# Kernel optimization log

Hardware: AMD Instinct MI355X
Metric: run time of the kernel (lower is better)

## Reference

```python
import jax, jax.numpy as jnp
import numpy as np
from functools import partial

VOCAB = 1000
HID = 512
EPS = 1e-3  # Keras BatchNorm default epsilon


def _conv1d(x, w, stride):
    # x: [B,T,C_in], w: [K,C_in,C_out]
    return jax.lax.conv_general_dilated(x, w, window_strides=(stride,), padding='SAME',
                                        dimension_numbers=('NWC', 'WIO', 'NWC'))


def setup_inputs() -> dict:
    key = jax.random.key(0)
    ks = jax.random.split(key, 8)
    s = lambda *sh: 1.0 / np.sqrt(sh[-2] if len(sh) > 1 else sh[-1])
    return {
        'x': jax.random.normal(ks[0], (32, 1600, 80), jnp.float32),
        'y_true': jax.random.randint(ks[1], (32, 201), 0, VOCAB),
        'bn_gamma': jnp.ones((80,), jnp.float32),
        'bn_beta': jnp.zeros((80,), jnp.float32),
        'conv0_w': jax.random.normal(ks[2], (5, 80, 512), jnp.float32) * 0.05,
        'conv0_b': jnp.zeros((512,), jnp.float32),
        'tcr_w': jax.random.normal(ks[3], (4, 5, 512, 512), jnp.float32) * 0.02,
        'tcr_b': jnp.zeros((4, 512), jnp.float32),
        'gru_kernel': jax.random.normal(ks[4], (VOCAB, 3 * HID), jnp.float32) * 0.03,
        'gru_rec_kernel': jax.random.normal(ks[5], (HID, 3 * HID), jnp.float32) * 0.04,
        'gru_bias': jnp.zeros((2, 3 * HID), jnp.float32),
        'fc_w': jax.random.normal(ks[6], (2 * HID, VOCAB), jnp.float32) * 0.03,
        'fc_b': jnp.zeros((VOCAB,), jnp.float32),
    }


def reference(x, y_true, bn_gamma, bn_beta, conv0_w, conv0_b, tcr_w, tcr_b,
              gru_kernel, gru_rec_kernel, gru_bias, fc_w, fc_b):
    # ---- Encoder ----
    # BatchNorm (training mode: batch statistics over batch & time)
    mean = jnp.mean(x, axis=(0, 1))
    var = jnp.var(x, axis=(0, 1))
    h = (x - mean) * jax.lax.rsqrt(var + EPS) * bn_gamma + bn_beta
    # strided Conv1D + relu -> [B, T=800, 512]
    h = jax.nn.relu(_conv1d(h, conv0_w, 2) + conv0_b)
    # Temporal conv residual blocks: out = relu(conv(x)) + x
    for i in range(tcr_w.shape[0]):
        h = jax.nn.relu(_conv1d(h, tcr_w[i], 1) + tcr_b[i]) + h
    enc = h  # [B, T, D]
    B = enc.shape[0]

    # ---- Decoder (teacher forcing, training branch) ----
    y_oh = jax.nn.one_hot(y_true, VOCAB, dtype=jnp.float32)  # [B, U+1, V]
    inputs = jnp.transpose(y_oh[:, :-1, :], (1, 0, 2))       # [U, B, V]
    bi, br = gru_bias[0], gru_bias[1]

    def step(hstate, y_u):
        # Keras GRUCell (reset_after=True)
        mx = y_u @ gru_kernel + bi
        mh = hstate @ gru_rec_kernel + br
        xz, xr, xh = jnp.split(mx, 3, axis=-1)
        hz, hr, hh = jnp.split(mh, 3, axis=-1)
        z = jax.nn.sigmoid(xz + hz)
        r = jax.nn.sigmoid(xr + hr)
        cand = jnp.tanh(xh + r * hh)
        h_new = z * hstate + (1.0 - z) * cand
        # Dot-product attention over encoder states
        scores = jnp.einsum('bd,btd->bt', h_new, enc)
        alpha = jax.nn.softmax(scores, axis=-1)
        ctx = jnp.einsum('bt,btd->bd', alpha, enc)
        # output projection with softmax activation
        y_pred = jax.nn.softmax(jnp.concatenate([h_new, ctx], axis=1) @ fc_w + fc_b, axis=-1)
        return h_new, y_pred

    h0 = jnp.zeros((B, HID), jnp.float32)
    _, outs = jax.lax.scan(step, h0, inputs)  # [U, B, V]
    return jnp.transpose(outs, (1, 0, 2))     # [B, U, V]
```

## Files before the change

### kernel.cpp

```cpp
#include <hip/hip_runtime.h>
#include <cstdint>

typedef _Float16 f16;
typedef __attribute__((ext_vector_type(2))) _Float16 f16x2;
typedef __attribute__((ext_vector_type(8))) _Float16 f16x8;
typedef __attribute__((ext_vector_type(4))) float f32x4;
typedef __attribute__((ext_vector_type(2))) float f32x2;
typedef __attribute__((ext_vector_type(8))) unsigned short us8;
typedef __attribute__((ext_vector_type(4))) int i32x4;

#define NB   32
#define TIN  1600
#define CIN  80
#define TOUT 800
#define DH   512
#define NV   1000
#define NU   200
#define TXP  1604
#define THP  804
#define EPSB 1e-3f
#define EWG  248

__device__ __forceinline__ void st_sys_f16(f16* p, float v)
{
    f16 h = (f16)v;
    short s; __builtin_memcpy(&s, &h, 2);
    int si = (int)s;
    asm volatile("global_store_short %0, %1, off sc0 sc1"
                 :: "v"(p), "v"(si) : "memory");
}

__device__ __forceinline__ void poll_h16(const f16* base, f16x8 v[16])
{
    while (true) {
        asm volatile(
            "global_load_dwordx4 %0, %16, off sc1\n\t"
            "global_load_dwordx4 %1, %16, off offset:64 sc1\n\t"
            "global_load_dwordx4 %2, %16, off offset:128 sc1\n\t"
            "global_load_dwordx4 %3, %16, off offset:192 sc1\n\t"
            "global_load_dwordx4 %4, %16, off offset:256 sc1\n\t"
            "global_load_dwordx4 %5, %16, off offset:320 sc1\n\t"
            "global_load_dwordx4 %6, %16, off offset:384 sc1\n\t"
            "global_load_dwordx4 %7, %16, off offset:448 sc1\n\t"
            "global_load_dwordx4 %8, %16, off offset:512 sc1\n\t"
            "global_load_dwordx4 %9, %16, off offset:576 sc1\n\t"
            "global_load_dwordx4 %10, %16, off offset:640 sc1\n\t"
            "global_load_dwordx4 %11, %16, off offset:704 sc1\n\t"
            "global_load_dwordx4 %12, %16, off offset:768 sc1\n\t"
            "global_load_dwordx4 %13, %16, off offset:832 sc1\n\t"
            "global_load_dwordx4 %14, %16, off offset:896 sc1\n\t"
            "global_load_dwordx4 %15, %16, off offset:960 sc1\n\t"
            "s_waitcnt vmcnt(0)"
            : "=&v"(v[0]), "=&v"(v[1]), "=&v"(v[2]), "=&v"(v[3]),
              "=&v"(v[4]), "=&v"(v[5]), "=&v"(v[6]), "=&v"(v[7]),
              "=&v"(v[8]), "=&v"(v[9]), "=&v"(v[10]), "=&v"(v[11]),
              "=&v"(v[12]), "=&v"(v[13]), "=&v"(v[14]), "=&v"(v[15])
            : "v"(base)
            : "memory");
        f16x8 s0 = v[0] + v[1],   s1 = v[2] + v[3];
        f16x8 s2 = v[4] + v[5],   s3 = v[6] + v[7];
        f16x8 s4 = v[8] + v[9],   s5 = v[10] + v[11];
        f16x8 s6 = v[12] + v[13], s7 = v[14] + v[15];
        s0 += s1; s2 += s3; s4 += s5; s6 += s7;
        s0 += s2; s4 += s6; s0 += s4;
        float r = (float)s0[0] + (float)s0[1] + (float)s0[2] + (float)s0[3]
                + (float)s0[4] + (float)s0[5] + (float)s0[6] + (float)s0[7];
        if (!__any(r != r)) return;
        __builtin_amdgcn_s_sleep(1);
    }
}

__device__ __forceinline__ float fast_tanh(float x)
{
    return 1.f - 2.f / (__expf(2.f * x) + 1.f);
}

__global__ void init_zero(float* gsum, float* gsumsq,
                          int* lcnt, f16* xpad, f16* hbufA, f16* hbufB,
                          f16* Hc)
{
    int tid = blockIdx.x * 256 + threadIdx.x;
    int stride = gridDim.x * 256;
    if (blockIdx.x == 0) {
        if (threadIdx.x < 80) { gsum[threadIdx.x] = 0.f; gsumsq[threadIdx.x] = 0.f; }
        if (threadIdx.x >= 128 && threadIdx.x < 136) lcnt[threadIdx.x - 128] = 0;
    }
    for (int i = tid; i < NB * 4 * CIN; i += stride) {
        int b = i / (4 * CIN), rr = (i / CIN) % 4, c = i % CIN;
        int row = (rr == 0) ? 0 : (1600 + rr);
        xpad[((long)b * TXP + row) * CIN + c] = (f16)0.f;
    }
    for (int i = tid; i < 2 * NB * 4 * DH; i += stride) {
        int q = i; int buf = q / (NB * 4 * DH); q %= NB * 4 * DH;
        int b = q / (4 * DH); int rr = (q / DH) % 4; int dd = q % DH;
        int row = (rr < 2) ? rr : (800 + rr);
        f16* hb = buf ? hbufB : hbufA;
        hb[((long)b * THP + row) * DH + dd] = (f16)0.f;
    }
    us8 sent;
#pragma unroll
    for (int e = 0; e < 8; e++) sent[e] = 0x7FFFu;
    for (int i = tid; i < 6400 * 64; i += stride)
        *(us8*)&Hc[(long)(i >> 6) * 1024 + (i & 63) * 8] = sent;
}

__global__ void transpose_f32_f16(const float* __restrict__ in, int R, int C,
                                  f16* __restrict__ out, int outRows, int outCols)
{
    __shared__ float t[32][33];
    int c0 = blockIdx.x * 32, r0 = blockIdx.y * 32;
    int x = threadIdx.x & 31, y = threadIdx.x >> 5;
    for (int i = y; i < 32; i += 8) {
        int r = r0 + i, c = c0 + x;
        t[i][x] = (r < R && c < C) ? in[(long)r * C + c] : 0.0f;
    }
    __syncthreads();
    for (int i = y; i < 32; i += 8) {
        int orow = c0 + i, ocol = r0 + x;
        if (orow < outRows && ocol < outCols)
            out[(long)orow * outCols + ocol] = (f16)t[x][i];
    }
}

__global__ void bn_stats(const float* __restrict__ x, float* gsum, float* gsumsq)
{
    __shared__ float ls[240], ls2[240];
    const float* base = x + (long)blockIdx.x * 200 * CIN;
    int tid = threadIdx.x;
    if (tid < 240) {
        int c = tid % 80, rg = tid / 80;
        float s = 0.f, s2 = 0.f;
        for (int r = rg; r < 200; r += 3) {
            float v = base[r * CIN + c];
            s += v; s2 += v * v;
        }
        ls[tid] = s; ls2[tid] = s2;
    }
    __syncthreads();
    if (tid < 80) {
        atomicAdd(&gsum[tid],   ls[tid] + ls[tid + 80] + ls[tid + 160]);
        atomicAdd(&gsumsq[tid], ls2[tid] + ls2[tid + 80] + ls2[tid + 160]);
    }
}

__global__ void bn_apply(const float* __restrict__ x, const float* __restrict__ gsum,
                         const float* __restrict__ gsumsq, const float* __restrict__ gamma,
                         const float* __restrict__ beta, f16* __restrict__ xpad)
{
    long idx = (long)blockIdx.x * 256 + threadIdx.x;
    if (idx >= (long)NB * TIN * CIN) return;
    int c = (int)(idx % CIN);
    long bt = idx / CIN;
    int t = (int)(bt % TIN); int b = (int)(bt / TIN);
    float mean = gsum[c] * (1.f / 51200.f);
    float var  = gsumsq[c] * (1.f / 51200.f) - mean * mean;
    float sc = gamma[c] * rsqrtf(var + EPSB);
    float sh = beta[c] - mean * sc;
    xpad[((long)b * TXP + t + 1) * CIN + c] = (f16)(x[idx] * sc + sh);
}

template<int MODE>
__launch_bounds__(256)
__global__ void gemm16(const f16* __restrict__ Ab, long strideA, long slabA,
                       const f16* __restrict__ Bb, long strideB, long slabB,
                       int M, int N, int Kchunks,
                       const float* __restrict__ bias,
                       float* __restrict__ outF)
{
    __shared__ f16 As[64][72];
    __shared__ f16 Bs[128][72];
    const int b = blockIdx.z;
    const f16* Abase = Ab + (long)b * slabA;
    const f16* Bbase = Bb + (long)b * slabB;
    const int m0 = blockIdx.x * 64, n0 = blockIdx.y * 128;
    const int tid = threadIdx.x;
    const int lane = tid & 63, wv = tid >> 6;
    const int lm = lane & 15, lk = lane >> 4;

    f32x4 vzero = {0.f, 0.f, 0.f, 0.f};
    f32x4 acc[4][2];
#pragma unroll
    for (int i = 0; i < 4; i++) { acc[i][0] = vzero; acc[i][1] = vzero; }

    const int srow = tid >> 3, scol = (tid & 7) * 8;

    for (int kc = 0; kc < Kchunks; kc++) {
        int kb = kc * 64;
#pragma unroll
        for (int p = 0; p < 2; p++) {
            int r = srow + p * 32;
            int m = m0 + r; if (m > M - 1) m = M - 1;
            *(us8*)&As[r][scol] = *(const us8*)(Abase + (long)m * strideA + kb + scol);
        }
#pragma unroll
        for (int p = 0; p < 4; p++) {
            int r = srow + p * 32;
            int n = n0 + r; if (n > N - 1) n = N - 1;
            *(us8*)&Bs[r][scol] = *(const us8*)(Bbase + (long)n * strideB + kb + scol);
        }
        __syncthreads();
#pragma unroll
        for (int ks = 0; ks < 2; ks++) {
            f16x8 af[4], bf[2];
#pragma unroll
            for (int mt = 0; mt < 4; mt++)
                af[mt] = *(const f16x8*)&As[mt * 16 + lm][ks * 32 + lk * 8];
#pragma unroll
            for (int nt = 0; nt < 2; nt++)
                bf[nt] = *(const f16x8*)&Bs[wv * 32 + nt * 16 + lm][ks * 32 + lk * 8];
#pragma unroll
            for (int mt = 0; mt < 4; mt++)
#pragma unroll
                for (int nt = 0; nt < 2; nt++)
                    acc[mt][nt] = __builtin_amdgcn_mfma_f32_16x16x32_f16(af[mt], bf[nt], acc[mt][nt], 0, 0, 0);
        }
        __syncthreads();
    }
#pragma unroll
    for (int mt = 0; mt < 4; mt++) {
#pragma unroll
        for (int nt = 0; nt < 2; nt++) {
            int n = n0 + wv * 32 + nt * 16 + lm;
#pragma unroll
            for (int reg = 0; reg < 4; reg++) {
                int m = m0 + mt * 16 + lk * 4 + reg;
                if (m >= M || n >= N) continue;
                float v = acc[mt][nt][reg];
                if (MODE == 2) {
                    outF[((long)b * NU + m) * 800 + n] = v;
                } else {
                    v += bias[n];
                    int u = m >> 5, bb = m & 31;
                    outF[((long)bb * NU + u) * 1000 + n] = v;
                }
            }
        }
    }
}

__device__ void enc_layer(int eb, int tid,
                          const f16* __restrict__ Ab, long strideA, long slabA,
                          const f16* __restrict__ Bb, long strideB,
                          int Kchunks, const float* __restrict__ bias,
                          const f16* __restrict__ resid, f16* __restrict__ outH,
                          long slabRO, f16 As[][72], f16 Bs[][72])
{
    const int lane = tid & 63, wv = tid >> 6;
    const int lm = lane & 15, lk = lane >> 4;
    const int srow = tid >> 3, scol = (tid & 7) * 8;
    f32x4 vzero = {0.f, 0.f, 0.f, 0.f};

    for (int t = eb; t < 1664; t += EWG) {
        int b = t / 52, rem = t - b * 52;
        int m0 = (rem >> 2) * 64, n0 = (rem & 3) * 128;
        const f16* Abase = Ab + (long)b * slabA;

        f32x4 acc[4][2];
#pragma unroll
        for (int i = 0; i < 4; i++) { acc[i][0] = vzero; acc[i][1] = vzero; }

        for (int kc = 0; kc < Kchunks; kc++) {
            int kb = kc * 64;
#pragma unroll
            for (int p = 0; p < 2; p++) {
                int r = srow + p * 32;
                int m = m0 + r; if (m > 799) m = 799;
                *(us8*)&As[r][scol] = *(const us8*)(Abase + (long)m * strideA + kb + scol);
            }
#pragma unroll
            for (int p = 0; p < 4; p++) {
                int r = srow + p * 32;
                *(us8*)&Bs[r][scol] = *(const us8*)(Bb + (long)(n0 + r) * strideB + kb + scol);
            }
            __syncthreads();
#pragma unroll
            for (int ks = 0; ks < 2; ks++) {
                f16x8 af[4], bf[2];
#pragma unroll
                for (int mt = 0; mt < 4; mt++)
                    af[mt] = *(const f16x8*)&As[mt * 16 + lm][ks * 32 + lk * 8];
#pragma unroll
                for (int nt = 0; nt < 2; nt++)
                    bf[nt] = *(const f16x8*)&Bs[wv * 32 + nt * 16 + lm][ks * 32 + lk * 8];
#pragma unroll
                for (int mt = 0; mt < 4; mt++)
#pragma unroll
                    for (int nt = 0; nt < 2; nt++)
                        acc[mt][nt] = __builtin_amdgcn_mfma_f32_16x16x32_f16(af[mt], bf[nt], acc[mt][nt], 0, 0, 0);
            }
            __syncthreads();
        }
#pragma unroll
        for (int mt = 0; mt < 4; mt++) {
#pragma unroll
            for (int nt = 0; nt < 2; nt++) {
                int n = n0 + wv * 32 + nt * 16 + lm;
#pragma unroll
                for (int reg = 0; reg < 4; reg++) {
                    int m = m0 + mt * 16 + lk * 4 + reg;
                    if (m >= 800) continue;
                    float v = acc[mt][nt][reg] + bias[n];
                    v = v > 0.f ? v : 0.f;
                    if (resid) v += (float)resid[(long)b * slabRO + (long)(2 + m) * DH + n];
                    outH[(long)b * slabRO + (long)(2 + m) * DH + n] = (f16)v;
                }
            }
        }
    }
}

__launch_bounds__(256, 1)
__global__ void enc_gru(const f16* __restrict__ wrecT, const float* __restrict__ gk,
                        const float* __restrict__ gbias, const int* __restrict__ ytrue,
                        f16* __restrict__ Hc,
                        const f16* __restrict__ xpad, const f16* __restrict__ w0T,
                        const float* __restrict__ b0, const f16* __restrict__ tcrT,
                        const float* __restrict__ tcrb,
                        f16* __restrict__ hbufA, f16* __restrict__ hbufB,
                        int* __restrict__ lcnt)
{
    const int tid = threadIdx.x;

    if (blockIdx.x < 8) {
        __shared__ int yl[NU * 32];
        const int lane = tid & 63, wv = tid >> 6;
        const int gw = (int)blockIdx.x * 4 + wv;
        const int lm = lane & 15, lk = lane >> 4;
        const int j = gw * 16 + lm;

        for (int i = tid; i < NU * 32; i += 256) {
            int b = i / NU, u = i - b * NU;
            yl[u * 32 + b] = ytrue[b * 201 + u];
        }

        f16x8 wf[3][16];
#pragma unroll
        for (int g = 0; g < 3; g++)
#pragma unroll
            for (int ks = 0; ks < 16; ks++) {
                wf[g][ks] = *(const f16x8*)&wrecT[(long)(g * 512 + j) * 512 + ks * 32 + lk * 8];
                asm volatile("" : "+v"(wf[g][ks]));
            }

        const float biz = gbias[j],        bir = gbias[512 + j],        bic = gbias[1024 + j];
        const float brz = gbias[1536 + j], brr = gbias[1536 + 512 + j], brc = gbias[1536 + 1024 + j];
        f32x4 vzero = {0.f, 0.f, 0.f, 0.f};

        __syncthreads();

        float hold[8];
        float nxz[8], nxr[8], nxh[8], mxz[8], mxr[8], mxh[8];
#pragma unroll
        for (int s = 0; s < 8; s++) {
            hold[s] = 0.f;
            int b = ((s >> 2) << 4) + lk * 4 + (s & 3);
            const float* gkr = gk + (long)yl[b] * 1536;
            nxz[s] = gkr[j]; nxr[s] = gkr[512 + j]; nxh[s] = gkr[1024 + j];
        }

        for (int u = 0; u < NU; u++) {
            int up = (u < NU - 1) ? u + 1 : u;
#pragma unroll
            for (int s = 0; s < 8; s++) {
                int b = ((s >> 2) << 4) + lk * 4 + (s & 3);
                const float* gkr = gk + (long)yl[up * 32 + b] * 1536;
                mxz[s] = gkr[j]; mxr[s] = gkr[512 + j]; mxh[s] = gkr[1024 + j];
            }

            f32x4 acc[3][2];
#pragma unroll
            for (int g = 0; g < 3; g++) { acc[g][0] = vzero; acc[g][1] = vzero; }

            if (u > 0) {
                const f16* baseA = Hc + ((long)(u - 1) * 32 + lm) * 1024 + lk * 8;
                {
                    f16x8 va[16];
                    poll_h16(baseA, va);
#pragma unroll
                    for (int ks = 0; ks < 16; ks++)
#pragma unroll
                        for (int g = 0; g < 3; g++)
                            acc[g][0] = __builtin_amdgcn_mfma_f32_16x16x32_f16(va[ks], wf[g][ks], acc[g][0], 0, 0, 0);
                }
                {
                    f16x8 vb[16];
                    poll_h16(baseA + 16 * 1024, vb);
#pragma unroll
                    for (int ks = 0; ks < 16; ks++)
#pragma unroll
                        for (int g = 0; g < 3; g++)
                            acc[g][1] = __builtin_amdgcn_mfma_f32_16x16x32_f16(vb[ks], wf[g][ks], acc[g][1], 0, 0, 0);
                }
            }

#pragma unroll
            for (int mt = 0; mt < 2; mt++) {
#pragma unroll
                for (int reg = 0; reg < 4; reg++) {
                    int s = mt * 4 + reg;
                    int b = mt * 16 + lk * 4 + reg;
                    float hz = acc[0][mt][reg] + brz;
                    float hr = acc[1][mt][reg] + brr;
                    float hh = acc[2][mt][reg] + brc;
                    float z = 1.f / (1.f + __expf(-(nxz[s] + biz + hz)));
                    float r = 1.f / (1.f + __expf(-(nxr[s] + bir + hr)));
                    float cd = fast_tanh(nxh[s] + bic + r * hh);
                    float hnew = z * hold[s] + (1.f - z) * cd;
                    hold[s] = hnew;
                    st_sys_f16(&Hc[((long)u * 32 + b) * 1024 + j], hnew);
                }
            }
#pragma unroll
            for (int s = 0; s < 8; s++) { nxz[s] = mxz[s]; nxr[s] = mxr[s]; nxh[s] = mxh[s]; }
        }
        asm volatile("s_waitcnt vmcnt(0)" ::: "memory");
        return;
    }

    __shared__ f16 As[64][72];
    __shared__ f16 Bs[128][72];
    const int eb = (int)blockIdx.x - 8;

    enc_layer(eb, tid, xpad, 160, (long)TXP * CIN, w0T, 448, 7, b0,
              nullptr, hbufA, (long)THP * DH, As, Bs);

    const f16* tin = hbufA; f16* tout = hbufB;
    for (int L = 0; L < 4; L++) {
        __syncthreads();
        if (tid == 0) {
            __hip_atomic_fetch_add(&lcnt[L], 1, __ATOMIC_RELEASE, __HIP_MEMORY_SCOPE_AGENT);
            while (__hip_atomic_load(&lcnt[L], __ATOMIC_RELAXED, __HIP_MEMORY_SCOPE_AGENT) < EWG)
                __builtin_amdgcn_s_sleep(8);
            (void)__hip_atomic_load(&lcnt[L], __ATOMIC_ACQUIRE, __HIP_MEMORY_SCOPE_AGENT);
        }
        __syncthreads();

        enc_layer(eb, tid, tin, 512, (long)THP * DH, tcrT + (size_t)L * 512 * 2560, 2560,
                  40, tcrb + L * 512, tin, tout, (long)THP * DH, As, Bs);
        const f16* t2 = tout; tout = (f16*)tin; tin = t2;
    }
}

__global__ void row_softmax(float* __restrict__ base, int len)
{
    float* s = base + (long)blockIdx.x * len;
    int tid = threadIdx.x;
    float v[4]; float mx = -1e30f;
#pragma unroll
    for (int i = 0; i < 4; i++) {
        int idx = tid + i * 256;
        v[i] = (idx < len) ? s[idx] : -1e30f;
        mx = fmaxf(mx, v[i]);
    }
#pragma unroll
    for (int off = 32; off; off >>= 1) mx = fmaxf(mx, __shfl_xor(mx, off));
    __shared__ float red[4], red2[4];
    if ((tid & 63) == 0) red[tid >> 6] = mx;
    __syncthreads();
    mx = fmaxf(fmaxf(red[0], red[1]), fmaxf(red[2], red[3]));
    float sum = 0.f;
#pragma unroll
    for (int i = 0; i < 4; i++) { v[i] = __expf(v[i] - mx); sum += v[i]; }
#pragma unroll
    for (int off = 32; off; off >>= 1) sum += __shfl_xor(sum, off);
    if ((tid & 63) == 0) red2[tid >> 6] = sum;
    __syncthreads();
    sum = red2[0] + red2[1] + red2[2] + red2[3];
    float inv = 1.f / sum;
#pragma unroll
    for (int i = 0; i < 4; i++) {
        int idx = tid + i * 256;
        if (idx < len) s[idx] = v[i] * inv;
    }
}

__launch_bounds__(256)
__global__ void attn_kernel(const f16* __restrict__ HcIn, const f16* __restrict__ enc,
                            f16* __restrict__ Hc)
{
    __shared__ float al[800][18];
    __shared__ float red[4], red2[4];
    const int b = blockIdx.x, ut = blockIdx.y;
    const int u0 = ut * 16;
    const int tid = threadIdx.x;
    const int lane = tid & 63, wv = tid >> 6;
    const int lm = lane & 15, lk = lane >> 4;

    int ua = u0 + lm; if (ua > NU - 1) ua = NU - 1;
    const f16* arow = HcIn + ((long)ua * 32 + b) * 1024 + lk * 8;
    f16x8 af[16];
#pragma unroll
    for (int kc = 0; kc < 16; kc++)
        af[kc] = *(const f16x8*)(arow + kc * 32);

    const f16* encb = enc + ((long)b * THP + 2) * DH;
    f32x4 vzero = {0.f, 0.f, 0.f, 0.f};
    for (int nt = wv; nt < 50; nt += 4) {
        const f16* brow = encb + (long)(nt * 16 + lm) * DH + lk * 8;
        f32x4 acc = vzero;
#pragma unroll
        for (int kc = 0; kc < 16; kc++) {
            f16x8 bf = *(const f16x8*)(brow + kc * 32);
            acc = __builtin_amdgcn_mfma_f32_16x16x32_f16(af[kc], bf, acc, 0, 0, 0);
        }
        const int t = nt * 16 + lm;
#pragma unroll
        for (int reg = 0; reg < 4; reg++)
            al[t][lk * 4 + reg] = acc[reg];
    }
    __syncthreads();

    for (int ul = 0; ul < 16; ul++) {
        int u = u0 + ul;
        if (u < NU) {
            float v[4]; float mx = -1e30f;
#pragma unroll
            for (int i = 0; i < 4; i++) {
                int idx = tid + i * 256;
                v[i] = (idx < 800) ? al[idx][ul] : -1e30f;
                mx = fmaxf(mx, v[i]);
            }
#pragma unroll
            for (int off = 32; off; off >>= 1) mx = fmaxf(mx, __shfl_xor(mx, off));
            if ((tid & 63) == 0) red[tid >> 6] = mx;
            __syncthreads();
            mx = fmaxf(fmaxf(red[0], red[1]), fmaxf(red[2], red[3]));
            float sum = 0.f;
#pragma unroll
            for (int i = 0; i < 4; i++) { v[i] = __expf(v[i] - mx); sum += v[i]; }
#pragma unroll
            for (int off = 32; off; off >>= 1) sum += __shfl_xor(sum, off);
            if ((tid & 63) == 0) red2[tid >> 6] = sum;
            __syncthreads();
            sum = red2[0] + red2[1] + red2[2] + red2[3];
            float inv = 1.f / sum;
#pragma unroll
            for (int i = 0; i < 4; i++) {
                int idx = tid + i * 256;
                if (idx < 800) al[idx][ul] = v[i] * inv;
            }
            __syncthreads();
        } else {
            for (int t = tid; t < 800; t += 256) al[t][ul] = 0.f;
        }
    }
    __syncthreads();

    int d0 = tid * 2;
    float a0[16], a1[16];
#pragma unroll
    for (int i = 0; i < 16; i++) { a0[i] = 0.f; a1[i] = 0.f; }
    const f16* encd = enc + ((long)b * THP + 2) * DH + d0;
    for (int t = 0; t < 800; t++) {
        f16x2 e = *(const f16x2*)&encd[(long)t * DH];
        float f0 = (float)e.x, f1 = (float)e.y;
#pragma unroll
        for (int g = 0; g < 8; g++) {
            f32x2 ap = *(const f32x2*)&al[t][2 * g];
            a0[2 * g]     += ap.x * f0; a0[2 * g + 1] += ap.y * f0;
            a1[2 * g]     += ap.x * f1; a1[2 * g + 1] += ap.y * f1;
        }
    }
#pragma unroll
    for (int ul = 0; ul < 16; ul++) {
        int u = u0 + ul;
        if (u < NU) {
            Hc[((long)u * 32 + b) * 1024 + 512 + d0]     = (f16)a0[ul];
            Hc[((long)u * 32 + b) * 1024 + 512 + d0 + 1] = (f16)a1[ul];
        }
    }
}

extern "C" void kernel_launch(void* const* d_in, const int* in_sizes, int n_in,
                              void* d_out, int out_size, void* d_ws, size_t ws_size,
                              hipStream_t stream)
{
    const float* x     = (const float*)d_in[0];
    const int*   ytrue = (const int*)d_in[1];
    const float* gamma = (const float*)d_in[2];
    const float* beta  = (const float*)d_in[3];
    const float* w0    = (const float*)d_in[4];
    const float* b0    = (const float*)d_in[5];
    const float* tcrw  = (const float*)d_in[6];
    const float* tcrb  = (const float*)d_in[7];
    const float* gk    = (const float*)d_in[8];
    const float* grk   = (const float*)d_in[9];
    const float* gbias = (const float*)d_in[10];
    const float* fcw   = (const float*)d_in[11];
    const float* fcb   = (const float*)d_in[12];
    float* out = (float*)d_out;
    (void)in_sizes; (void)n_in; (void)out_size; (void)ws_size;

    char* ws = (char*)d_ws;
    size_t o = 0;
    auto alloc = [&](size_t bytes) { size_t r = o; o += (bytes + 255) & ~(size_t)255; return r; };
    f16*   xpad   = (f16*)(ws + alloc((size_t)NB * TXP * CIN * 2));
    f16*   hbufA  = (f16*)(ws + alloc((size_t)NB * THP * DH * 2));
    f16*   hbufB  = (f16*)(ws + alloc((size_t)NB * THP * DH * 2));
    f16*   Hc     = (f16*)(ws + alloc((size_t)NU * NB * 1024 * 2));
    f16*   w0T    = (f16*)(ws + alloc((size_t)512 * 448 * 2));
    f16*   tcrT   = (f16*)(ws + alloc((size_t)4 * 512 * 2560 * 2));
    f16*   wrecT  = (f16*)(ws + alloc((size_t)1536 * 512 * 2));
    f16*   fcT    = (f16*)(ws + alloc((size_t)1024 * 1024 * 2));
    float* gsum   = (float*)(ws + alloc(80 * 4));
    float* gsumsq = (float*)(ws + alloc(80 * 4));
    int*   lcnt   = (int*)(ws + alloc(64));

    init_zero<<<64, 256, 0, stream>>>(gsum, gsumsq, lcnt, xpad, hbufA, hbufB, Hc);
    transpose_f32_f16<<<dim3(16, 14), 256, 0, stream>>>(w0, 400, 512, w0T, 512, 448);
    for (int i = 0; i < 4; i++)
        transpose_f32_f16<<<dim3(16, 80), 256, 0, stream>>>(tcrw + (size_t)i * 2560 * 512, 2560, 512,
                                                            tcrT + (size_t)i * 512 * 2560, 512, 2560);
    transpose_f32_f16<<<dim3(48, 16), 256, 0, stream>>>(grk, 512, 1536, wrecT, 1536, 512);
    transpose_f32_f16<<<dim3(32, 32), 256, 0, stream>>>(fcw, 1024, 1000, fcT, 1024, 1024);

    bn_stats<<<256, 256, 0, stream>>>(x, gsum, gsumsq);
    bn_apply<<<16000, 256, 0, stream>>>(x, gsum, gsumsq, gamma, beta, xpad);

    enc_gru<<<8 + EWG, 256, 0, stream>>>(wrecT, gk, gbias, ytrue, Hc,
                                         xpad, w0T, b0, tcrT, tcrb, hbufA, hbufB, lcnt);
    const f16* enc = hbufA;

    attn_kernel<<<dim3(32, 13), 256, 0, stream>>>(Hc, enc, Hc);

    gemm16<3><<<dim3(100, 8, 1), 256, 0, stream>>>(Hc, 1024, 0, fcT, 1024, 0,
        6400, 1000, 16, fcb, out);
    row_softmax<<<6400, 256, 0, stream>>>(out, 1000);
}
```

Baseline: 1.671 ms.

## Fuse attention and output projection into persistent encoder/GRU kernel with work queue

```diff
diff --git a/kernel.cpp b/kernel.cpp
--- a/kernel.cpp
+++ b/kernel.cpp
@@ -20,6 +20,7 @@
 #define THP  804
 #define EPSB 1e-3f
 #define EWG  248
+#define NITEM (13 * 32)
 
 __device__ __forceinline__ void st_sys_f16(f16* p, float v)
 {
@@ -30,6 +31,7 @@
                  :: "v"(p), "v"(si) : "memory");
 }
 
+template<int SLEEP>
 __device__ __forceinline__ void poll_h16(const f16* base, f16x8 v[16])
 {
     while (true) {
@@ -66,7 +68,7 @@
         float r = (float)s0[0] + (float)s0[1] + (float)s0[2] + (float)s0[3]
                 + (float)s0[4] + (float)s0[5] + (float)s0[6] + (float)s0[7];
         if (!__any(r != r)) return;
-        __builtin_amdgcn_s_sleep(1);
+        __builtin_amdgcn_s_sleep(SLEEP);
     }
 }
 
@@ -83,7 +85,7 @@
     int stride = gridDim.x * 256;
     if (blockIdx.x == 0) {
         if (threadIdx.x < 80) { gsum[threadIdx.x] = 0.f; gsumsq[threadIdx.x] = 0.f; }
-        if (threadIdx.x >= 128 && threadIdx.x < 136) lcnt[threadIdx.x - 128] = 0;
+        if (threadIdx.x >= 128 && threadIdx.x < 144) lcnt[threadIdx.x - 128] = 0;
     }
     for (int i = tid; i < NB * 4 * CIN; i += stride) {
         int b = i / (4 * CIN), rr = (i / CIN) % 4, c = i % CIN;
@@ -159,85 +161,6 @@
     xpad[((long)b * TXP + t + 1) * CIN + c] = (f16)(x[idx] * sc + sh);
 }
 
-template<int MODE>
-__launch_bounds__(256)
-__global__ void gemm16(const f16* __restrict__ Ab, long strideA, long slabA,
-                       const f16* __restrict__ Bb, long strideB, long slabB,
-                       int M, int N, int Kchunks,
-                       const float* __restrict__ bias,
-                       float* __restrict__ outF)
-{
-    __shared__ f16 As[64][72];
-    __shared__ f16 Bs[128][72];
-    const int b = blockIdx.z;
-    const f16* Abase = Ab + (long)b * slabA;
-    const f16* Bbase = Bb + (long)b * slabB;
-    const int m0 = blockIdx.x * 64, n0 = blockIdx.y * 128;
-    const int tid = threadIdx.x;
-    const int lane = tid & 63, wv = tid >> 6;
-    const int lm = lane & 15, lk = lane >> 4;
-
-    f32x4 vzero = {0.f, 0.f, 0.f, 0.f};
-    f32x4 acc[4][2];
-#pragma unroll
-    for (int i = 0; i < 4; i++) { acc[i][0] = vzero; acc[i][1] = vzero; }
-
-    const int srow = tid >> 3, scol = (tid & 7) * 8;
-
-    for (int kc = 0; kc < Kchunks; kc++) {
-        int kb = kc * 64;
-#pragma unroll
-        for (int p = 0; p < 2; p++) {
-            int r = srow + p * 32;
-            int m = m0 + r; if (m > M - 1) m = M - 1;
-            *(us8*)&As[r][scol] = *(const us8*)(Abase + (long)m * strideA + kb + scol);
-        }
-#pragma unroll
-        for (int p = 0; p < 4; p++) {
-            int r = srow + p * 32;
-            int n = n0 + r; if (n > N - 1) n = N - 1;
-            *(us8*)&Bs[r][scol] = *(const us8*)(Bbase + (long)n * strideB + kb + scol);
-        }
-        __syncthreads();
-#pragma unroll
-        for (int ks = 0; ks < 2; ks++) {
-            f16x8 af[4], bf[2];
-#pragma unroll
-            for (int mt = 0; mt < 4; mt++)
-                af[mt] = *(const f16x8*)&As[mt * 16 + lm][ks * 32 + lk * 8];
-#pragma unroll
-            for (int nt = 0; nt < 2; nt++)
-                bf[nt] = *(const f16x8*)&Bs[wv * 32 + nt * 16 + lm][ks * 32 + lk * 8];
-#pragma unroll
-            for (int mt = 0; mt < 4; mt++)
-#pragma unroll
-                for (int nt = 0; nt < 2; nt++)
-                    acc[mt][nt] = __builtin_amdgcn_mfma_f32_16x16x32_f16(af[mt], bf[nt], acc[mt][nt], 0, 0, 0);
-        }
-        __syncthreads();
-    }
-#pragma unroll
-    for (int mt = 0; mt < 4; mt++) {
-#pragma unroll
-        for (int nt = 0; nt < 2; nt++) {
-            int n = n0 + wv * 32 + nt * 16 + lm;
-#pragma unroll
-            for (int reg = 0; reg < 4; reg++) {
-                int m = m0 + mt * 16 + lk * 4 + reg;
-                if (m >= M || n >= N) continue;
-                float v = acc[mt][nt][reg];
-                if (MODE == 2) {
-                    outF[((long)b * NU + m) * 800 + n] = v;
-                } else {
-                    v += bias[n];
-                    int u = m >> 5, bb = m & 31;
-                    outF[((long)bb * NU + u) * 1000 + n] = v;
-                }
-            }
-        }
-    }
-}
-
 __device__ void enc_layer(int eb, int tid,
                           const f16* __restrict__ Ab, long strideA, long slabA,
                           const f16* __restrict__ Bb, long strideB,
@@ -317,12 +240,15 @@
                         const float* __restrict__ b0, const f16* __restrict__ tcrT,
                         const float* __restrict__ tcrb,
                         f16* __restrict__ hbufA, f16* __restrict__ hbufB,
-                        int* __restrict__ lcnt)
-{
+                        int* __restrict__ lcnt,
+                        const f16* __restrict__ fcT, const float* __restrict__ fcb,
+                        float* __restrict__ out)
+{
+    __shared__ __align__(16) char smem[57664];
     const int tid = threadIdx.x;
 
     if (blockIdx.x < 8) {
-        __shared__ int yl[NU * 32];
+        int* yl = (int*)smem;
         const int lane = tid & 63, wv = tid >> 6;
         const int gw = (int)blockIdx.x * 4 + wv;
         const int lm = lane & 15, lk = lane >> 4;
@@ -375,7 +301,7 @@
                 const f16* baseA = Hc + ((long)(u - 1) * 32 + lm) * 1024 + lk * 8;
                 {
                     f16x8 va[16];
-                    poll_h16(baseA, va);
+                    poll_h16<1>(baseA, va);
 #pragma unroll
                     for (int ks = 0; ks < 16; ks++)
 #pragma unroll
@@ -384,7 +310,7 @@
                 }
                 {
                     f16x8 vb[16];
-                    poll_h16(baseA + 16 * 1024, vb);
+                    poll_h16<1>(baseA + 16 * 1024, vb);
 #pragma unroll
                     for (int ks = 0; ks < 16; ks++)
 #pragma unroll
@@ -417,9 +343,12 @@
         return;
     }
 
-    __shared__ f16 As[64][72];
-    __shared__ f16 Bs[128][72];
+    f16 (*As)[72] = (f16(*)[72])smem;
+    f16 (*Bs)[72] = (f16(*)[72])(smem + 64 * 72 * 2);
     const int eb = (int)blockIdx.x - 8;
+    const int lane = tid & 63, wv = tid >> 6;
+    const int lm = lane & 15, lk = lane >> 4;
+    f32x4 vzero = {0.f, 0.f, 0.f, 0.f};
 
     enc_layer(eb, tid, xpad, 160, (long)TXP * CIN, w0T, 448, 7, b0,
               nullptr, hbufA, (long)THP * DH, As, Bs);
@@ -438,6 +367,140 @@
         enc_layer(eb, tid, tin, 512, (long)THP * DH, tcrT + (size_t)L * 512 * 2560, 2560,
                   40, tcrb + L * 512, tin, tout, (long)THP * DH, As, Bs);
         const f16* t2 = tout; tout = (f16*)tin; tin = t2;
+    }
+
+    __syncthreads();
+    if (tid == 0) {
+        __hip_atomic_fetch_add(&lcnt[4], 1, __ATOMIC_RELEASE, __HIP_MEMORY_SCOPE_AGENT);
+        while (__hip_atomic_load(&lcnt[4], __ATOMIC_RELAXED, __HIP_MEMORY_SCOPE_AGENT) < EWG)
+            __builtin_amdgcn_s_sleep(8);
+        (void)__hip_atomic_load(&lcnt[4], __ATOMIC_ACQUIRE, __HIP_MEMORY_SCOPE_AGENT);
+    }
+    __syncthreads();
+
+    const f16* enc = hbufA;
+    float (*al)[18] = (float(*)[18])smem;
+    float* red  = (float*)(smem + 57600);
+    float* red2 = (float*)(smem + 57616);
+    int*   itemP = (int*)(smem + 57632);
+    f16*   ctxT = (f16*)smem;
+
+    while (true) {
+        __syncthreads();
+        if (tid == 0)
+            *itemP = __hip_atomic_fetch_add(&lcnt[8], 1, __ATOMIC_RELAXED, __HIP_MEMORY_SCOPE_AGENT);
+        __syncthreads();
+        const int item = *itemP;
+        if (item >= NITEM) break;
+        const int ut = item >> 5, b = item & 31;
+        const int u0 = ut * 16;
+
+        int ua = u0 + lm; if (ua > NU - 1) ua = NU - 1;
+        f16x8 af[16];
+        poll_h16<32>(Hc + ((long)ua * 32 + b) * 1024 + lk * 8, af);
+
+        const f16* encb = enc + ((long)b * THP + 2) * DH;
+        for (int nt = wv; nt < 50; nt += 4) {
+            const f16* brow = encb + (long)(nt * 16 + lm) * DH + lk * 8;
+            f32x4 acc = vzero;
+#pragma unroll
+            for (int kc = 0; kc < 16; kc++) {
+                f16x8 bf = *(const f16x8*)(brow + kc * 32);
+                acc = __builtin_amdgcn_mfma_f32_16x16x32_f16(af[kc], bf, acc, 0, 0, 0);
+            }
+            const int t = nt * 16 + lm;
+#pragma unroll
+            for (int reg = 0; reg < 4; reg++)
+                al[t][lk * 4 + reg] = acc[reg];
+        }
+        __syncthreads();
+
+        for (int ul = 0; ul < 16; ul++) {
+            int u = u0 + ul;
+            if (u < NU) {
+                float v[4]; float mx = -1e30f;
+#pragma unroll
+                for (int i = 0; i < 4; i++) {
+                    int idx = tid + i * 256;
+                    v[i] = (idx < 800) ? al[idx][ul] : -1e30f;
+                    mx = fmaxf(mx, v[i]);
+                }
+#pragma unroll
+                for (int off = 32; off; off >>= 1) mx = fmaxf(mx, __shfl_xor(mx, off));
+                if ((tid & 63) == 0) red[tid >> 6] = mx;
+                __syncthreads();
+                mx = fmaxf(fmaxf(red[0], red[1]), fmaxf(red[2], red[3]));
+                float sum = 0.f;
+#pragma unroll
+                for (int i = 0; i < 4; i++) { v[i] = __expf(v[i] - mx); sum += v[i]; }
+#pragma unroll
+                for (int off = 32; off; off >>= 1) sum += __shfl_xor(sum, off);
+                if ((tid & 63) == 0) red2[tid >> 6] = sum;
+                __syncthreads();
+                float s = red2[0] + red2[1] + red2[2] + red2[3];
+                float inv = 1.f / s;
+#pragma unroll
+                for (int i = 0; i < 4; i++) {
+                    int idx = tid + i * 256;
+                    if (idx < 800) al[idx][ul] = v[i] * inv;
+                }
+                __syncthreads();
+            } else {
+                for (int t = tid; t < 800; t += 256) al[t][ul] = 0.f;
+            }
+        }
+        __syncthreads();
+
+        int d0 = tid * 2;
+        float a0[16], a1[16];
+#pragma unroll
+        for (int i = 0; i < 16; i++) { a0[i] = 0.f; a1[i] = 0.f; }
+        const f16* encd = enc + ((long)b * THP + 2) * DH + d0;
+        for (int t = 0; t < 800; t++) {
+            f16x2 e = *(const f16x2*)&encd[(long)t * DH];
+            float f0 = (float)e.x, f1 = (float)e.y;
+#pragma unroll
+            for (int g = 0; g < 8; g++) {
+                f32x2 ap = *(const f32x2*)&al[t][2 * g];
+                a0[2 * g]     += ap.x * f0; a0[2 * g + 1] += ap.y * f0;
+                a1[2 * g]     += ap.x * f1; a1[2 * g + 1] += ap.y * f1;
+            }
+        }
+        __syncthreads();
+
+#pragma unroll
+        for (int ul = 0; ul < 16; ul++) {
+            ctxT[ul * 520 + d0]     = (f16)a0[ul];
+            ctxT[ul * 520 + d0 + 1] = (f16)a1[ul];
+        }
+        __syncthreads();
+
+        f16x8 cf[16];
+#pragma unroll
+        for (int kc = 0; kc < 16; kc++)
+            cf[kc] = *(const f16x8*)&ctxT[lm * 520 + kc * 32 + lk * 8];
+
+        for (int nt = wv; nt < 63; nt += 4) {
+            const int n0 = nt * 16;
+            const f16* brow = fcT + (long)(n0 + lm) * 1024 + lk * 8;
+            f32x4 acc = vzero;
+#pragma unroll
+            for (int kc = 0; kc < 16; kc++) {
+                f16x8 bf = *(const f16x8*)(brow + kc * 32);
+                acc = __builtin_amdgcn_mfma_f32_16x16x32_f16(af[kc], bf, acc, 0, 0, 0);
+            }
+#pragma unroll
+            for (int kc = 0; kc < 16; kc++) {
+                f16x8 bf = *(const f16x8*)(brow + 512 + kc * 32);
+                acc = __builtin_amdgcn_mfma_f32_16x16x32_f16(cf[kc], bf, acc, 0, 0, 0);
+            }
+#pragma unroll
+            for (int reg = 0; reg < 4; reg++) {
+                int u = u0 + lk * 4 + reg, n = n0 + lm;
+                if (u < NU && n < 1000)
+                    out[((long)b * NU + u) * 1000 + n] = acc[reg] + fcb[n];
+            }
+        }
     }
 }
 
@@ -471,103 +534,6 @@
     for (int i = 0; i < 4; i++) {
         int idx = tid + i * 256;
         if (idx < len) s[idx] = v[i] * inv;
-    }
-}
-
-__launch_bounds__(256)
-__global__ void attn_kernel(const f16* __restrict__ HcIn, const f16* __restrict__ enc,
-                            f16* __restrict__ Hc)
-{
-    __shared__ float al[800][18];
-    __shared__ float red[4], red2[4];
-    const int b = blockIdx.x, ut = blockIdx.y;
-    const int u0 = ut * 16;
-    const int tid = threadIdx.x;
-    const int lane = tid & 63, wv = tid >> 6;
-    const int lm = lane & 15, lk = lane >> 4;
-
-    int ua = u0 + lm; if (ua > NU - 1) ua = NU - 1;
-    const f16* arow = HcIn + ((long)ua * 32 + b) * 1024 + lk * 8;
-    f16x8 af[16];
-#pragma unroll
-    for (int kc = 0; kc < 16; kc++)
-        af[kc] = *(const f16x8*)(arow + kc * 32);
-
-    const f16* encb = enc + ((long)b * THP + 2) * DH;
-    f32x4 vzero = {0.f, 0.f, 0.f, 0.f};
-    for (int nt = wv; nt < 50; nt += 4) {
-        const f16* brow = encb + (long)(nt * 16 + lm) * DH + lk * 8;
-        f32x4 acc = vzero;
-#pragma unroll
-        for (int kc = 0; kc < 16; kc++) {
-            f16x8 bf = *(const f16x8*)(brow + kc * 32);
-            acc = __builtin_amdgcn_mfma_f32_16x16x32_f16(af[kc], bf, acc, 0, 0, 0);
-        }
-        const int t = nt * 16 + lm;
-#pragma unroll
-        for (int reg = 0; reg < 4; reg++)
-            al[t][lk * 4 + reg] = acc[reg];
-    }
-    __syncthreads();
-
-    for (int ul = 0; ul < 16; ul++) {
-        int u = u0 + ul;
-        if (u < NU) {
-            float v[4]; float mx = -1e30f;
-#pragma unroll
-            for (int i = 0; i < 4; i++) {
-                int idx = tid + i * 256;
-                v[i] = (idx < 800) ? al[idx][ul] : -1e30f;
-                mx = fmaxf(mx, v[i]);
-            }
-#pragma unroll
-            for (int off = 32; off; off >>= 1) mx = fmaxf(mx, __shfl_xor(mx, off));
-            if ((tid & 63) == 0) red[tid >> 6] = mx;
-            __syncthreads();
-            mx = fmaxf(fmaxf(red[0], red[1]), fmaxf(red[2], red[3]));
-            float sum = 0.f;
-#pragma unroll
-            for (int i = 0; i < 4; i++) { v[i] = __expf(v[i] - mx); sum += v[i]; }
-#pragma unroll
-            for (int off = 32; off; off >>= 1) sum += __shfl_xor(sum, off);
-            if ((tid & 63) == 0) red2[tid >> 6] = sum;
-            __syncthreads();
-            sum = red2[0] + red2[1] + red2[2] + red2[3];
-            float inv = 1.f / sum;
-#pragma unroll
-            for (int i = 0; i < 4; i++) {
-                int idx = tid + i * 256;
-                if (idx < 800) al[idx][ul] = v[i] * inv;
-            }
-            __syncthreads();
-        } else {
-            for (int t = tid; t < 800; t += 256) al[t][ul] = 0.f;
-        }
-    }
-    __syncthreads();
-
-    int d0 = tid * 2;
-    float a0[16], a1[16];
-#pragma unroll
-    for (int i = 0; i < 16; i++) { a0[i] = 0.f; a1[i] = 0.f; }
-    const f16* encd = enc + ((long)b * THP + 2) * DH + d0;
-    for (int t = 0; t < 800; t++) {
-        f16x2 e = *(const f16x2*)&encd[(long)t * DH];
-        float f0 = (float)e.x, f1 = (float)e.y;
-#pragma unroll
-        for (int g = 0; g < 8; g++) {
-            f32x2 ap = *(const f32x2*)&al[t][2 * g];
-            a0[2 * g]     += ap.x * f0; a0[2 * g + 1] += ap.y * f0;
-            a1[2 * g]     += ap.x * f1; a1[2 * g + 1] += ap.y * f1;
-        }
-    }
-#pragma unroll
-    for (int ul = 0; ul < 16; ul++) {
-        int u = u0 + ul;
-        if (u < NU) {
-            Hc[((long)u * 32 + b) * 1024 + 512 + d0]     = (f16)a0[ul];
-            Hc[((long)u * 32 + b) * 1024 + 512 + d0 + 1] = (f16)a1[ul];
-        }
     }
 }
 
@@ -618,12 +584,8 @@
     bn_apply<<<16000, 256, 0, stream>>>(x, gsum, gsumsq, gamma, beta, xpad);
 
     enc_gru<<<8 + EWG, 256, 0, stream>>>(wrecT, gk, gbias, ytrue, Hc,
-                                         xpad, w0T, b0, tcrT, tcrb, hbufA, hbufB, lcnt);
-    const f16* enc = hbufA;
-
-    attn_kernel<<<dim3(32, 13), 256, 0, stream>>>(Hc, enc, Hc);
-
-    gemm16<3><<<dim3(100, 8, 1), 256, 0, stream>>>(Hc, 1024, 0, fcT, 1024, 0,
-        6400, 1000, 16, fcb, out);
+                                         xpad, w0T, b0, tcrT, tcrb, hbufA, hbufB, lcnt,
+                                         fcT, fcb, out);
+
     row_softmax<<<6400, 256, 0, stream>>>(out, 1000);
 }
```

Result: slower. 1.812 ms (+8.4%).
